# Kernel tuning notes

Hardware: AMD Instinct MI355X
Metric: run time of the kernel (lower is better)

The kernel has to match this reference:

```python
import jax, jax.numpy as jnp
import numpy as np
from jax import lax

Q = 3          # Self-ONN polynomial order
EPS = 1e-5     # InstanceNorm1d eps


def setup_inputs() -> dict:
    key = jax.random.key(0)
    k1, k2, k3 = jax.random.split(key, 3)
    B, Cin, L = 16, 128, 8192
    Cout, K = 128, 3
    x = jax.random.normal(k1, (B, Cin, L), dtype=jnp.float32)
    # Conv1d weight over power-expanded channels: [Cout, Cin*Q, K]
    W = jax.random.normal(k2, (Cout, Cin * Q, K), dtype=jnp.float32) * 0.05
    b = jax.random.normal(k3, (Cout,), dtype=jnp.float32) * 0.05
    return {"x": x, "W": W, "b": b}


def reference(x, W, b):
    x = jnp.repeat(x, 2, axis=-1)
    # Self-ONN power expansion: concat x^1..x^Q along channel dim -> (B, C*Q, 2L)
    powers = jnp.concatenate([x ** (i + 1) for i in range(Q)], axis=1)
    # Conv1d, stride 1, padding 1 (same length)
    out = lax.conv_general_dilated(
        powers, W,
        window_strides=(1,),
        padding=[(1, 1)],
        dimension_numbers=("NCH", "OIH", "NCH"),
    ) + b[None, :, None]
    # InstanceNorm1d (affine=False): normalize over length per (batch, channel)
    mean = jnp.mean(out, axis=-1, keepdims=True)
    var = jnp.var(out, axis=-1, keepdims=True)
    out = (out - mean) * lax.rsqrt(var + EPS)
    # Tanh activation (self.relu is nn.Tanh()); dropout=False -> no-op
    return jnp.tanh(out)
```

## Files before the change

### kernel.cpp

```cpp
#include <hip/hip_runtime.h>
#include <hip/hip_fp16.h>
#include <math.h>

#define BATCH 16
#define CIN   128
#define LIN   8192
#define COUT  128
#define LOUT  16384
#define KEXP  768
#define NT    128
#define NTILES (LIN/NT)
#define PCOLS 130
#define PCPAD 136
#define PSZ   (PCOLS*PCPAD)

typedef _Float16 f16x8 __attribute__((ext_vector_type(8)));
typedef float    f32x4 __attribute__((ext_vector_type(4)));

__global__ void prep_weights(const float* __restrict__ W,
                             _Float16* __restrict__ WE,
                             _Float16* __restrict__ WO) {
  int idx = blockIdx.x * 256 + threadIdx.x;
  int co = idx / KEXP;
  int k  = idx % KEXP;
  int sh = (k >= 384) ? 1 : 0;
  int cq = k - 384 * sh;
  const float* w = W + ((size_t)co * 384 + cq) * 3;
  float we, wo;
  if (sh == 0) { we = w[0];        wo = w[0] + w[1]; }
  else         { we = w[1] + w[2]; wo = w[2];        }
  int q  = cq >> 7;
  int c  = cq & 127;
  int ks = q * 8 + sh * 4 + (c >> 5);
  int kk = c & 31, quad = kk >> 3, j = kk & 7;
  int mtile = co >> 4, l15 = co & 15;
  size_t off = ((size_t)((mtile * 24 + ks) * 64) + quad * 16 + l15) * 8 + j;
  WE[off] = (_Float16)we;
  WO[off] = (_Float16)wo;
}

__launch_bounds__(512, 4)
__global__ void conv_gemm(const float* __restrict__ x,
                          const _Float16* __restrict__ WE,
                          const _Float16* __restrict__ WO,
                          float* __restrict__ out,
                          float* __restrict__ stats) {
  extern __shared__ char smem[];
  float*    sstats = (float*)smem;
  _Float16* plane  = (_Float16*)(smem + 1024);

  const int tile = blockIdx.x;
  const int b    = blockIdx.y;
  const int i0   = tile * NT;
  const int t    = threadIdx.x;
  const int lane = t & 63;
  const int wave = t >> 6;
  const int p    = wave >> 1;
  const int isO  = wave & 1;
  const int wm   = p >> 1, wn = p & 1;
  const int l15  = lane & 15, quad = lane >> 4;
  const int kl   = quad * 8;

  if (t < 128) { sstats[2 * t] = 0.f; sstats[2 * t + 1] = 0.f; }

  const float* xb = x + (size_t)b * CIN * LIN;
  const _Float16* Wsel = isO ? WO : WE;

  f32x4 acc[4][4];
  const f32x4 zero = {0.f, 0.f, 0.f, 0.f};
#pragma unroll
  for (int fm = 0; fm < 4; ++fm)
#pragma unroll
    for (int fn = 0; fn < 4; ++fn) acc[fm][fn] = zero;

#pragma unroll
  for (int q = 0; q < 3; ++q) {
    for (int task = t; task < PCOLS * 16; task += 512) {
      int g   = task / PCOLS;
      int col = task - g * PCOLS;
      int c8  = g * 8;
      int gi  = i0 - 1 + col;
      bool ok = (gi >= 0 && gi < LIN);
      f16x8 w;
#pragma unroll
      for (int j = 0; j < 8; ++j) {
        float v = ok ? xb[(size_t)(c8 + j) * LIN + gi] : 0.f;
        float pv = (q == 0) ? v : ((q == 1) ? v * v : v * v * v);
        w[j] = (_Float16)pv;
      }
      *(f16x8*)(plane + col * PCPAD + c8) = w;
    }
    __syncthreads();

#pragma unroll
    for (int s = 0; s < 8; ++s) {
      const int cb   = (s & 3) * 32;
      const int shft = (s >> 2) + isO;
      const _Float16* pb = plane + cb + kl;
      f16x8 bf[4], af[4];
#pragma unroll
      for (int fn = 0; fn < 4; ++fn) {
        int colB = wn * 64 + fn * 16 + l15 + shft;
        bf[fn] = *(const f16x8*)(pb + colB * PCPAD);
      }
#pragma unroll
      for (int fm = 0; fm < 4; ++fm) {
        int mt = wm * 4 + fm;
        af[fm] = *(const f16x8*)(Wsel + ((size_t)((mt * 24 + q * 8 + s) * 64) + lane) * 8);
      }
#pragma unroll
      for (int fm = 0; fm < 4; ++fm)
#pragma unroll
        for (int fn = 0; fn < 4; ++fn)
          acc[fm][fn] = __builtin_amdgcn_mfma_f32_16x16x32_f16(af[fm], bf[fn], acc[fm][fn], 0, 0, 0);
    }
    __syncthreads();
  }

  float* orow_base = out + (size_t)b * COUT * LOUT + isO;
#pragma unroll
  for (int fm = 0; fm < 4; ++fm) {
#pragma unroll
    for (int r = 0; r < 4; ++r) {
      float s1 = 0.f, s2 = 0.f;
#pragma unroll
      for (int fn = 0; fn < 4; ++fn) {
        float v = acc[fm][fn][r];
        s1 += v;
        s2 += v * v;
      }
#pragma unroll
      for (int off = 8; off >= 1; off >>= 1) {
        s1 += __shfl_xor(s1, off, 64);
        s2 += __shfl_xor(s2, off, 64);
      }
      int co = wm * 64 + fm * 16 + quad * 4 + r;
      if (l15 == 0) {
        atomicAdd(&sstats[2 * co], s1);
        atomicAdd(&sstats[2 * co + 1], s2);
      }
      float* orow = orow_base + (size_t)co * LOUT;
#pragma unroll
      for (int fn = 0; fn < 4; ++fn) {
        int n = i0 + wn * 64 + fn * 16 + l15;
        orow[2 * n] = acc[fm][fn][r];
      }
    }
  }
  __syncthreads();
  if (t < 128) {
    atomicAdd(&stats[((size_t)b * COUT + t) * 2],     sstats[2 * t]);
    atomicAdd(&stats[((size_t)b * COUT + t) * 2 + 1], sstats[2 * t + 1]);
  }
}

__device__ inline float tanh_fast(float z) {
  float e = __expf(2.f * z);
  return 1.f - 2.f * __builtin_amdgcn_rcpf(e + 1.f);
}

__global__ void norm_tanh(float* __restrict__ out, const float* __restrict__ stats) {
  int row = blockIdx.x;
  float s1 = stats[2 * row], s2 = stats[2 * row + 1];
  const float invN = 1.f / (float)LOUT;
  float mean = s1 * invN;
  float var  = fmaxf(s2 * invN - mean * mean, 0.f);
  float inv  = rsqrtf(var + 1e-5f);
  float c0   = -mean * inv;
  float4* p = (float4*)(out + (size_t)row * LOUT);
  for (int i = threadIdx.x; i < LOUT / 4; i += 256) {
    float4 v = p[i];
    v.x = tanh_fast(fmaf(v.x, inv, c0));
    v.y = tanh_fast(fmaf(v.y, inv, c0));
    v.z = tanh_fast(fmaf(v.z, inv, c0));
    v.w = tanh_fast(fmaf(v.w, inv, c0));
    p[i] = v;
  }
}

extern "C" void kernel_launch(void* const* d_in, const int* in_sizes, int n_in,
                              void* d_out, int out_size, void* d_ws, size_t ws_size,
                              hipStream_t stream) {
  const float* x = (const float*)d_in[0];
  const float* W = (const float*)d_in[1];
  float* out = (float*)d_out;

  float*    stats = (float*)d_ws;
  _Float16* WE    = (_Float16*)((char*)d_ws + 16384);
  _Float16* WO    = WE + (size_t)COUT * KEXP;

  hipMemsetAsync(d_ws, 0, 16384, stream);
  prep_weights<<<dim3((COUT * KEXP) / 256), dim3(256), 0, stream>>>(W, WE, WO);

  size_t shmem = 1024 + (size_t)PSZ * 2;
  hipFuncSetAttribute(reinterpret_cast<const void*>(conv_gemm),
                      hipFuncAttributeMaxDynamicSharedMemorySize, (int)shmem);
  conv_gemm<<<dim3(NTILES, BATCH), dim3(512), shmem, stream>>>(x, WE, WO, out, stats);

  norm_tanh<<<dim3(BATCH * COUT), dim3(256), 0, stream>>>(out, stats);
}
```

Baseline: 312.2 us.

## Double the length tile and double-buffer power planes to overlap build with MFMA

```diff
diff --git a/kernel.cpp b/kernel.cpp
--- a/kernel.cpp
+++ b/kernel.cpp
@@ -8,9 +8,9 @@
 #define COUT  128
 #define LOUT  16384
 #define KEXP  768
-#define NT    128
+#define NT    256
 #define NTILES (LIN/NT)
-#define PCOLS 130
+#define PCOLS 258
 #define PCPAD 136
 #define PSZ   (PCOLS*PCPAD)
 
@@ -39,7 +39,7 @@
   WO[off] = (_Float16)wo;
 }
 
-__launch_bounds__(512, 4)
+__launch_bounds__(512, 2)
 __global__ void conv_gemm(const float* __restrict__ x,
                           const _Float16* __restrict__ WE,
                           const _Float16* __restrict__ WO,
@@ -47,7 +47,8 @@
                           float* __restrict__ stats) {
   extern __shared__ char smem[];
   float*    sstats = (float*)smem;
-  _Float16* plane  = (_Float16*)(smem + 1024);
+  _Float16* P0     = (_Float16*)(smem + 1024);
+  _Float16* P1     = P0 + PSZ;
 
   const int tile = blockIdx.x;
   const int b    = blockIdx.y;
@@ -66,56 +67,69 @@
   const float* xb = x + (size_t)b * CIN * LIN;
   const _Float16* Wsel = isO ? WO : WE;
 
-  f32x4 acc[4][4];
+  f32x4 acc[4][8];
   const f32x4 zero = {0.f, 0.f, 0.f, 0.f};
 #pragma unroll
   for (int fm = 0; fm < 4; ++fm)
 #pragma unroll
-    for (int fn = 0; fn < 4; ++fn) acc[fm][fn] = zero;
-
-#pragma unroll
-  for (int q = 0; q < 3; ++q) {
-    for (int task = t; task < PCOLS * 16; task += 512) {
-      int g   = task / PCOLS;
-      int col = task - g * PCOLS;
-      int c8  = g * 8;
-      int gi  = i0 - 1 + col;
-      bool ok = (gi >= 0 && gi < LIN);
-      f16x8 w;
-#pragma unroll
-      for (int j = 0; j < 8; ++j) {
-        float v = ok ? xb[(size_t)(c8 + j) * LIN + gi] : 0.f;
-        float pv = (q == 0) ? v : ((q == 1) ? v * v : v * v * v);
-        w[j] = (_Float16)pv;
-      }
-      *(f16x8*)(plane + col * PCPAD + c8) = w;
+    for (int fn = 0; fn < 8; ++fn) acc[fm][fn] = zero;
+
+  auto build = [&](int qp, _Float16* dst) {
+    for (int it = 0; it < 9; ++it) {
+      int idx = it * 512 + t;
+      if (idx < PCOLS * 16) {
+        int g   = idx / PCOLS;
+        int col = idx - g * PCOLS;
+        int c8  = g * 8;
+        int gi  = i0 - 1 + col;
+        bool ok = (gi >= 0 && gi < LIN);
+        f16x8 w;
+#pragma unroll
+        for (int j = 0; j < 8; ++j) {
+          float v = ok ? xb[(size_t)(c8 + j) * LIN + gi] : 0.f;
+          float pv = (qp == 1) ? v : ((qp == 2) ? v * v : v * v * v);
+          w[j] = (_Float16)pv;
+        }
+        *(f16x8*)(dst + col * PCPAD + c8) = w;
+      }
     }
-    __syncthreads();
-
+  };
+
+  auto ksteps = [&](int q, const _Float16* pl) {
 #pragma unroll
     for (int s = 0; s < 8; ++s) {
       const int cb   = (s & 3) * 32;
       const int shft = (s >> 2) + isO;
-      const _Float16* pb = plane + cb + kl;
-      f16x8 bf[4], af[4];
-#pragma unroll
-      for (int fn = 0; fn < 4; ++fn) {
-        int colB = wn * 64 + fn * 16 + l15 + shft;
-        bf[fn] = *(const f16x8*)(pb + colB * PCPAD);
-      }
+      const _Float16* pb = pl + cb + kl;
+      f16x8 af[4], bf[8];
 #pragma unroll
       for (int fm = 0; fm < 4; ++fm) {
         int mt = wm * 4 + fm;
         af[fm] = *(const f16x8*)(Wsel + ((size_t)((mt * 24 + q * 8 + s) * 64) + lane) * 8);
       }
 #pragma unroll
+      for (int fn = 0; fn < 8; ++fn) {
+        int colB = wn * 128 + fn * 16 + l15 + shft;
+        bf[fn] = *(const f16x8*)(pb + colB * PCPAD);
+      }
+#pragma unroll
       for (int fm = 0; fm < 4; ++fm)
 #pragma unroll
-        for (int fn = 0; fn < 4; ++fn)
+        for (int fn = 0; fn < 8; ++fn)
           acc[fm][fn] = __builtin_amdgcn_mfma_f32_16x16x32_f16(af[fm], bf[fn], acc[fm][fn], 0, 0, 0);
     }
-    __syncthreads();
-  }
+  };
+
+  build(1, P0);
+  __syncthreads();
+  build(2, P1);
+  ksteps(0, P0);
+  __syncthreads();
+  build(3, P0);
+  ksteps(1, P1);
+  __syncthreads();
+  ksteps(2, P0);
+  __syncthreads();
 
   float* orow_base = out + (size_t)b * COUT * LOUT + isO;
 #pragma unroll
@@ -124,7 +138,7 @@
     for (int r = 0; r < 4; ++r) {
       float s1 = 0.f, s2 = 0.f;
 #pragma unroll
-      for (int fn = 0; fn < 4; ++fn) {
+      for (int fn = 0; fn < 8; ++fn) {
         float v = acc[fm][fn][r];
         s1 += v;
         s2 += v * v;
@@ -141,8 +155,8 @@
       }
       float* orow = orow_base + (size_t)co * LOUT;
 #pragma unroll
-      for (int fn = 0; fn < 4; ++fn) {
-        int n = i0 + wn * 64 + fn * 16 + l15;
+      for (int fn = 0; fn < 8; ++fn) {
+        int n = i0 + wn * 128 + fn * 16 + l15;
         orow[2 * n] = acc[fm][fn][r];
       }
     }
@@ -192,7 +206,7 @@
   hipMemsetAsync(d_ws, 0, 16384, stream);
   prep_weights<<<dim3((COUT * KEXP) / 256), dim3(256), 0, stream>>>(W, WE, WO);
 
-  size_t shmem = 1024 + (size_t)PSZ * 2;
+  size_t shmem = 1024 + (size_t)2 * PSZ * 2;
   hipFuncSetAttribute(reinterpret_cast<const void*>(conv_gemm),
                       hipFuncAttributeMaxDynamicSharedMemorySize, (int)shmem);
   conv_gemm<<<dim3(NTILES, BATCH), dim3(512), shmem, stream>>>(x, WE, WO, out, stats);
```

Result: slower. 341.7 us (+9.4%).
